# Kernel optimization log

Measured on AMD Instinct MI355X. Metric: run time of the kernel, lower is better.

The kernel has to match this reference:

```python
import jax, jax.numpy as jnp
import numpy as np

N = 10000          # nodes
E = 200000         # edges (avg degree 20)
LAT = 128          # latent dim
NEXP = 8           # experts
NTYPE = 95         # atom types (hard-coded 95x0e in module)
M0, M1, M2 = 128, 64, 32          # node/out irreps muls for l=0,1,2 (dim 480)
E0, E1, E2 = 64, 32, 16           # edge irreps muls (dim 240)
C0, C1, C2 = M0 + E0, M1 + E1, M2 + E2   # concat channels per l
T0 = M0 + M1 + M2                 # gate-input scalars: 128 scalars + 96 gates
AVG_NEIGH = 20.0


def setup_inputs() -> dict:
    key = jax.random.key(0)
    ks = jax.random.split(key, 32)
    r = lambda i, sh: jax.random.normal(ks[i], sh, dtype=jnp.float32)
    return {
        "latents": r(0, (E, LAT)),
        "node_features": r(1, (N, M0 + 3 * M1 + 5 * M2)),
        "edge_features": r(2, (E, E0 + 3 * E1 + 5 * E2)),
        "edge_vector": r(3, (E, 3)),
        "mole_globals": r(4, (LAT,)),
        "wigner_D1": r(5, (E, 3, 3)),
        "wigner_D2": r(6, (E, 5, 5)),
        "node_onehot": jax.nn.one_hot(jax.random.randint(ks[7], (N,), 0, NTYPE), NTYPE, dtype=jnp.float32),
        "Wg": r(8, (LAT, NEXP)),
        "Wm": r(9, (LAT, NEXP)),
        "W0_e": r(10, (NEXP, C0, T0)), "W0_s": r(11, (C0, T0)),
        "W1_e": r(12, (NEXP, C1, M1)), "W1_s": r(13, (C1, M1)),
        "W2_e": r(14, (NEXP, C2, M2)), "W2_s": r(15, (C2, M2)),
        "Wp0": r(16, (M0, M0)), "bp0": jnp.zeros((M0,), jnp.float32),
        "Wp1": r(17, (M1, M1)), "Wp2": r(18, (M2, M2)),
        "Wenv": r(19, (LAT, M0 + M1 + M2)),
        "Woh0": r(20, (M0, NTYPE)), "Woh1": r(21, (M1, NTYPE)), "Woh2": r(22, (M2, NTYPE)),
        "atom_type": jax.random.randint(ks[23], (N,), 0, NTYPE),
        "edge_index": jax.random.randint(ks[24], (2, E), 0, N),
        "active_edges": jnp.arange(E),
    }


def _mix(x, We, Ws, g):
    """Latent(expert)-conditioned per-l channel mixing: y = x @ (sum_e g_e W_e + W_shared).
    Loops over the small fixed expert count; never materializes per-edge weight matrices."""
    xm = x if x.ndim == 3 else x[:, :, None]           # [a, c, m]
    y = jnp.einsum('acm,co->aom', xm, Ws)
    for e in range(NEXP):
        y = y + g[:, e, None, None] * jnp.einsum('acm,co->aom', xm, We[e])
    y = y * float(1.0 / np.sqrt(xm.shape[1]))
    return y[:, :, 0] if x.ndim == 2 else y


def reference(latents, node_features, edge_features, edge_vector, mole_globals,
              wigner_D1, wigner_D2, node_onehot, Wg, Wm,
              W0_e, W0_s, W1_e, W1_s, W2_e, W2_s,
              Wp0, bp0, Wp1, Wp2, Wenv, Woh0, Woh1, Woh2,
              atom_type, edge_index, active_edges):
    edge_center = edge_index[0][active_edges]
    lat = latents[active_edges]
    # gather node features along edges, split irreps blocks
    xn = node_features[edge_center]                         # [Ea, 480]
    n0 = xn[:, :M0]
    n1 = xn[:, M0:M0 + 3 * M1].reshape(-1, M1, 3)
    n2 = xn[:, M0 + 3 * M1:].reshape(-1, M2, 5)
    e0 = edge_features[:, :E0]
    e1 = edge_features[:, E0:E0 + 3 * E1].reshape(-1, E1, 3)
    e2 = edge_features[:, E0 + 3 * E1:].reshape(-1, E2, 5)
    x0 = jnp.concatenate([n0, e0], axis=1)                  # [Ea, C0]
    x1 = jnp.concatenate([n1, e1], axis=1)                  # [Ea, C1, 3]
    x2 = jnp.concatenate([n2, e2], axis=1)                  # [Ea, C2, 5]
    # latent + molecular-global conditioned expert gates
    gates = jax.nn.softmax(lat @ Wg + mole_globals @ Wm, axis=-1)   # [Ea, NEXP]
    # SO(2)-style TP: rotate l>0 blocks into edge frame (Wigner-D), mix channels, rotate back
    x1r = jnp.einsum('amn,acn->acm', wigner_D1, x1)
    x2r = jnp.einsum('amn,acn->acm', wigner_D2, x2)
    t0 = _mix(x0, W0_e, W0_s, gates)                        # [Ea, T0]
    t1 = jnp.einsum('anm,aom->aon', wigner_D1, _mix(x1r, W1_e, W1_s, gates))
    t2 = jnp.einsum('anm,aom->aon', wigner_D2, _mix(x2r, W2_e, W2_s, gates))
    # Gate nonlinearity: silu scalars, sigmoid gates scale l>0 channels
    s = jax.nn.silu(t0[:, :M0])
    v1 = t1 * jax.nn.sigmoid(t0[:, M0:M0 + M1])[:, :, None]
    v2 = t2 * jax.nn.sigmoid(t0[:, M0 + M1:])[:, :, None]
    # lin_post: per-l equivariant linear (bias only on scalars), fan-in normalized
    s = s @ Wp0 * float(1.0 / np.sqrt(M0)) + bp0
    v1 = jnp.einsum('acm,co->aom', v1, Wp1) * float(1.0 / np.sqrt(M1))
    v2 = jnp.einsum('acm,co->aom', v2, Wp2) * float(1.0 / np.sqrt(M2))
    # E3ElementLinear: per-channel weights generated from latents
    w = lat @ Wenv * float(1.0 / np.sqrt(LAT))              # [Ea, M0+M1+M2]
    s = s * w[:, :M0]
    v1 = v1 * w[:, M0:M0 + M1, None]
    v2 = v2 * w[:, M0 + M1:, None]
    # scatter-reduce messages to nodes, normalize by rsqrt(avg_num_neighbors)
    norm = float(1.0 / np.sqrt(AVG_NEIGH))
    o0 = jax.ops.segment_sum(s, edge_center, num_segments=N) * norm
    o1 = jax.ops.segment_sum(v1, edge_center, num_segments=N) * norm
    o2 = jax.ops.segment_sum(v2, edge_center, num_segments=N) * norm
    # residual blend (res_update_params=0 -> u=sigmoid(0)=0.5), identity residual
    u = 0.5
    c_old = float(1.0 / np.sqrt(u * u + 1.0))
    c_new = u * c_old
    h0 = c_old * node_features[:, :M0] + c_new * o0
    h1 = c_old * node_features[:, M0:M0 + 3 * M1].reshape(N, M1, 3) + c_new * o1
    h2 = c_old * node_features[:, M0 + 3 * M1:].reshape(N, M2, 5) + c_new * o2
    # layer-onehot 'uvu' weighted TP with 95x0e, fan-in normalized, added residually
    invs = float(1.0 / np.sqrt(NTYPE))
    h0 = h0 + h0 * (node_onehot @ Woh0.T) * invs
    h1 = h1 + h1 * (node_onehot @ Woh1.T)[:, :, None] * invs
    h2 = h2 + h2 * (node_onehot @ Woh2.T)[:, :, None] * invs
    return jnp.concatenate([h0, h1.reshape(N, 3 * M1), h2.reshape(N, 5 * M2)], axis=1)
```

## Files before the change

kernel.cpp:

```cpp
#include <hip/hip_runtime.h>
#include <math.h>

namespace {

typedef __attribute__((ext_vector_type(8))) short short8;
typedef __attribute__((ext_vector_type(4))) float f32x4;

constexpr int kN   = 10000;
constexpr int kE   = 200000;
constexpr int kNT  = 95;
constexpr int kNFD = 480;

__device__ __forceinline__ ushort bf(float f) {
  union { float f; uint u; } c; c.f = f;
  uint r = c.u + 0x7FFF + ((c.u >> 16) & 1);
  return (ushort)(r >> 16);
}
__device__ __forceinline__ float fb(ushort u) {
  union { uint u; float f; } c; c.u = ((uint)u) << 16;
  return c.f;
}
__device__ __forceinline__ uint pk2(float a, float b) {
  return (uint)bf(a) | ((uint)bf(b) << 16);
}

__device__ __forceinline__ void fastbar() {
  asm volatile("s_waitcnt lgkmcnt(0)" ::: "memory");
  __builtin_amdgcn_s_barrier();
}

__device__ __forceinline__ void packone(int u, const float* We, const float* Ws,
                                        int expStride, int Kreal, int Nstride,
                                        int Nreal, int NT, int NKp, ushort* d) {
  int i = u & 7;
  int lane = (u >> 3) & 63;
  int rest = u >> 9;
  int kc = rest % NKp; rest /= NKp;
  int nt = rest % NT;
  int e  = rest / NT;
  int k = kc*32 + (lane >> 4)*8 + i;
  int n = nt*16 + (lane & 15);
  float v = 0.f;
  if (k < Kreal && n < Nreal) {
    const float* s = (Ws != nullptr && e == 8) ? Ws : (We + (size_t)e*expStride);
    v = s[(size_t)k*Nstride + n];
  }
  d[u] = bf(v);
}

constexpr int PK0   = 0;
constexpr int PK1   = 442368;
constexpr int PK2   = 497664;
constexpr int PKENV = 516096;
constexpr int PKP0  = 544768;
constexpr int PKP1  = 561152;
constexpr int PKP2  = 565248;
constexpr int PKTOT = 566272;

__global__ __launch_bounds__(256)
void pack_k(const float* __restrict__ W0e, const float* __restrict__ W0s,
            const float* __restrict__ W1e, const float* __restrict__ W1s,
            const float* __restrict__ W2e, const float* __restrict__ W2s,
            const float* __restrict__ Wenv, const float* __restrict__ Wp0,
            const float* __restrict__ Wp1, const float* __restrict__ Wp2,
            ushort* __restrict__ dst) {
  int gid = blockIdx.x*256 + threadIdx.x;
  if (gid >= PKTOT) return;
  if (gid < PK1)        packone(gid - PK0,   W0e, W0s, 192*224, 192, 224, 224, 16, 6, dst + PK0);
  else if (gid < PK2)   packone(gid - PK1,   W1e, W1s, 96*64,    96,  64,  64,  4, 3, dst + PK1);
  else if (gid < PKENV) packone(gid - PK2,   W2e, W2s, 48*32,    48,  32,  32,  2, 2, dst + PK2);
  else if (gid < PKP0)  packone(gid - PKENV, Wenv, nullptr, 0,  128, 224, 224, 14, 4, dst + PKENV);
  else if (gid < PKP1)  packone(gid - PKP0,  Wp0, nullptr, 0,   128, 128, 128,  8, 4, dst + PKP0);
  else if (gid < PKP2)  packone(gid - PKP1,  Wp1, nullptr, 0,    64,  64,  64,  4, 2, dst + PKP1);
  else                  packone(gid - PKP2,  Wp2, nullptr, 0,    32,  32,  32,  2, 1, dst + PKP2);
}

__global__ __launch_bounds__(64)
void mgl_k(const float* __restrict__ mgv, const float* __restrict__ Wm,
           float* __restrict__ mgl) {
  int x = threadIdx.x;
  if (x < 8) {
    float s = 0.f;
    for (int l = 0; l < 128; ++l) s += mgv[l]*Wm[l*8 + x];
    mgl[x] = s;
  }
}

__global__ __launch_bounds__(256)
void hist_k(const int* __restrict__ eidx, const int* __restrict__ act,
            int* __restrict__ counts) {
  int e = blockIdx.x*256 + threadIdx.x;
  if (e < kE) atomicAdd(&counts[eidx[act[e]]], 1);
}

__global__ __launch_bounds__(256)
void scan_k(const int* __restrict__ counts, int* __restrict__ rowptr,
            int* __restrict__ cursor) {
  __shared__ int part[256];
  const int t = threadIdx.x;
  const int start = t*40;
  int local = 0;
  for (int i = 0; i < 40; ++i) {
    int idx = start + i;
    if (idx < kN) local += counts[idx];
  }
  part[t] = local;
  __syncthreads();
  for (int ofs = 1; ofs < 256; ofs <<= 1) {
    int v = (t >= ofs) ? part[t - ofs] : 0;
    __syncthreads();
    part[t] += v;
    __syncthreads();
  }
  int run = part[t] - local;
  for (int i = 0; i < 40; ++i) {
    int idx = start + i;
    if (idx < kN) {
      rowptr[idx] = run;
      cursor[idx] = run;
      run += counts[idx];
    }
  }
  if (t == 255) rowptr[kN] = run;
}

__global__ __launch_bounds__(256)
void scatter_k(const int* __restrict__ eidx, const int* __restrict__ act,
               int* __restrict__ cursor, int* __restrict__ elist) {
  int e = blockIdx.x*256 + threadIdx.x;
  if (e < kE) {
    int n = eidx[act[e]];
    int pos = atomicAdd(&cursor[n], 1);
    elist[pos] = e;
  }
}

__global__ __launch_bounds__(256)
void prep_k(const float* __restrict__ latents, const float* __restrict__ nodef,
            const float* __restrict__ edgef, const float* __restrict__ mgl,
            const float* __restrict__ D1, const float* __restrict__ D2,
            const float* __restrict__ Wg,
            const int* __restrict__ eidx, const int* __restrict__ act,
            float* __restrict__ coefg,
            ushort* __restrict__ x0, ushort* __restrict__ x1r,
            ushort* __restrict__ x2r) {
  __shared__ int aidl[32], cenl[32];
  const int tid = threadIdx.x;
  const int base = blockIdx.x*32;

  if (tid < 32) {
    int a = act[base + tid];
    aidl[tid] = a;
    cenl[tid] = eidx[a];
  }
  __syncthreads();

  {
    int e = tid >> 3, x = tid & 7;
    const float* lat = latents + (size_t)aidl[e]*128;
    float s = mgl[x];
    for (int l = 0; l < 128; ++l) s += lat[l]*Wg[l*8 + x];
    float mx = s;
    mx = fmaxf(mx, __shfl_xor(mx, 1));
    mx = fmaxf(mx, __shfl_xor(mx, 2));
    mx = fmaxf(mx, __shfl_xor(mx, 4));
    float ex = __expf(s - mx);
    float sm = ex;
    sm += __shfl_xor(sm, 1);
    sm += __shfl_xor(sm, 2);
    sm += __shfl_xor(sm, 4);
    size_t a = base + e;
    coefg[a*9 + x] = ex/sm;
    if (x == 0) coefg[a*9 + 8] = 1.f;
  }

  for (int u = tid; u < 32*24; u += 256) {
    int e = u/24, g = u - e*24;
    int c0 = g*8;
    size_t a = base + e;
    const float* s = (g < 16) ? (nodef + (size_t)cenl[e]*kNFD + c0)
                              : (edgef + a*240 + (c0 - 128));
    float4 f0 = *(const float4*)s;
    float4 f1 = *(const float4*)(s + 4);
    uint4 o;
    o.x = pk2(f0.x, f0.y); o.y = pk2(f0.z, f0.w);
    o.z = pk2(f1.x, f1.y); o.w = pk2(f1.z, f1.w);
    *(uint4*)(x0 + a*192 + c0) = o;
  }

  for (int u = tid; u < 32*36; u += 256) {
    int e = u/36, r = u - e*36;
    int mm = r/12, g = r - mm*12;
    int c0 = g*8;
    size_t a = base + e;
    const float* dd = D1 + a*9 + mm*3;
    const float* s = (g < 8) ? (nodef + (size_t)cenl[e]*kNFD + 128 + c0*3)
                             : (edgef + a*240 + 64 + (c0 - 64)*3);
    float ld[24];
    #pragma unroll
    for (int q = 0; q < 6; ++q)
      *(float4*)(ld + q*4) = *(const float4*)(s + q*4);
    float d0 = dd[0], d1 = dd[1], d2 = dd[2];
    float ov[8];
    #pragma unroll
    for (int j = 0; j < 8; ++j)
      ov[j] = d0*ld[3*j] + d1*ld[3*j + 1] + d2*ld[3*j + 2];
    uint4 o;
    o.x = pk2(ov[0], ov[1]); o.y = pk2(ov[2], ov[3]);
    o.z = pk2(ov[4], ov[5]); o.w = pk2(ov[6], ov[7]);
    *(uint4*)(x1r + (a*3 + mm)*96 + c0) = o;
  }

  for (int u = tid; u < 32*40; u += 256) {
    int e = u/40, r = u - e*40;
    int mm = r >> 3, g = r & 7;
    int c0 = g*8;
    size_t a = base + e;
    uint4 o = {0u,0u,0u,0u};
    if (g < 6) {
      const float* dd = D2 + a*25 + mm*5;
      const float* s = (g < 4) ? (nodef + (size_t)cenl[e]*kNFD + 320 + c0*5)
                               : (edgef + a*240 + 160 + (c0 - 32)*5);
      float ld[40];
      #pragma unroll
      for (int q = 0; q < 10; ++q)
        *(float4*)(ld + q*4) = *(const float4*)(s + q*4);
      float d0 = dd[0], d1 = dd[1], d2 = dd[2], d3 = dd[3], d4 = dd[4];
      float ov[8];
      #pragma unroll
      for (int j = 0; j < 8; ++j)
        ov[j] = d0*ld[5*j] + d1*ld[5*j+1] + d2*ld[5*j+2] + d3*ld[5*j+3] + d4*ld[5*j+4];
      o.x = pk2(ov[0], ov[1]); o.y = pk2(ov[2], ov[3]);
      o.z = pk2(ov[4], ov[5]); o.w = pk2(ov[6], ov[7]);
    }
    *(uint4*)(x2r + (a*5 + mm)*64 + c0) = o;
  }
}

constexpr int gemm_smbytes(int K1, int NK, int N, int NEXP) {
  int LDA = K1 + 8;
  int NT = N/16;
  int a = 128*LDA*2;
  int b = NT*NK*1024;
  int u = a > b ? a : b;
  return u + (NEXP > 1 ? 128*NEXP*4 : 0);
}

template<int DIV, int K1, int NK, int N, int NEXP, int EPI, bool AF32>
__global__ __launch_bounds__(512)
void gemm_k(const ushort* __restrict__ A, const float* __restrict__ Af,
            const int* __restrict__ ridx, int strideA,
            const ushort* __restrict__ Bpk, const float* __restrict__ coefg,
            int rowsReal, float norm,
            ushort* __restrict__ outbf, const float* __restrict__ bias,
            const ushort* __restrict__ wenvbf, int WCOL) {
  constexpr int NT  = N/16;
  constexpr int CTW = NT/2;
  constexpr int LDA = K1 + 8;
  constexpr int ABYTES = 128*LDA*2;
  constexpr int BBYTES = NT*NK*1024;
  constexpr int UNI = (ABYTES > BBYTES) ? ABYTES : BBYTES;

  extern __shared__ char smraw[];
  ushort* Asm = (ushort*)smraw;
  float* coefsm = (float*)(smraw + UNI);

  const int tid = threadIdx.x;
  const int row0 = blockIdx.x*128;

  constexpr int C8 = K1/8;
  for (int u = tid; u < 128*C8; u += 512) {
    int r = u / C8, c8 = u - r*C8;
    int gr = row0 + r;
    uint4 v = {0u,0u,0u,0u};
    if (gr < rowsReal) {
      if constexpr (AF32) {
        const float* s = Af + (size_t)(ridx ? ridx[gr] : gr)*strideA + c8*8;
        float4 f0 = *(const float4*)s;
        float4 f1 = *(const float4*)(s + 4);
        v.x = pk2(f0.x, f0.y); v.y = pk2(f0.z, f0.w);
        v.z = pk2(f1.x, f1.y); v.w = pk2(f1.z, f1.w);
      } else {
        v = *(const uint4*)(A + (size_t)gr*strideA + c8*8);
      }
    }
    *(uint4*)(&Asm[r*LDA + c8*8]) = v;
  }
  if constexpr (NEXP > 1) {
    for (int u = tid; u < 128*NEXP; u += 512) {
      int r = u / NEXP, e = u - r*NEXP;
      int a = (row0 + r)/DIV;
      coefsm[r*NEXP + e] = coefg[(size_t)a*NEXP + e];
    }
  }
  __syncthreads();

  const int lane = tid & 63, wid = tid >> 6;
  const int cg = wid & 1, rg = wid >> 1;
  const int rbase = rg*32;
  const int lrow = lane & 15, lkb = lane >> 4;

  short8 af[2][NK];
  #pragma unroll
  for (int rt = 0; rt < 2; ++rt)
    #pragma unroll
    for (int kc = 0; kc < NK; ++kc)
      af[rt][kc] = *(const short8*)(&Asm[(rbase + rt*16 + lrow)*LDA + kc*32 + lkb*8]);

  f32x4 acc[2][CTW];
  #pragma unroll
  for (int rt = 0; rt < 2; ++rt)
    #pragma unroll
    for (int ct = 0; ct < CTW; ++ct)
      acc[rt][ct] = f32x4{0.f,0.f,0.f,0.f};

  __syncthreads();

  union BU { uint4 u; short8 s; };
  uint4* Bsm4 = (uint4*)smraw;
  const uint4* Bg4 = (const uint4*)Bpk;

  for (int e = 0; e < NEXP; ++e) {
    for (int u = tid; u < NT*NK*64; u += 512)
      Bsm4[u] = Bg4[(size_t)e*(NT*NK*64) + u];
    __syncthreads();

    if constexpr (NEXP > 1) {
      float cf[2][4];
      #pragma unroll
      for (int rt = 0; rt < 2; ++rt)
        #pragma unroll
        for (int q = 0; q < 4; ++q)
          cf[rt][q] = coefsm[(rbase + rt*16 + lkb*4 + q)*NEXP + e];
      #pragma unroll
      for (int ct = 0; ct < CTW; ++ct) {
        int nt = cg*CTW + ct;
        f32x4 z[2];
        z[0] = f32x4{0.f,0.f,0.f,0.f};
        z[1] = f32x4{0.f,0.f,0.f,0.f};
        #pragma unroll
        for (int kc = 0; kc < NK; ++kc) {
          BU b; b.u = Bsm4[(nt*NK + kc)*64 + lane];
          z[0] = __builtin_amdgcn_mfma_f32_16x16x32_bf16(af[0][kc], b.s, z[0], 0, 0, 0);
          z[1] = __builtin_amdgcn_mfma_f32_16x16x32_bf16(af[1][kc], b.s, z[1], 0, 0, 0);
        }
        #pragma unroll
        for (int q = 0; q < 4; ++q) {
          acc[0][ct][q] += cf[0][q]*z[0][q];
          acc[1][ct][q] += cf[1][q]*z[1][q];
        }
      }
    } else {
      #pragma unroll
      for (int ct = 0; ct < CTW; ++ct) {
        int nt = cg*CTW + ct;
        #pragma unroll
        for (int kc = 0; kc < NK; ++kc) {
          BU b; b.u = Bsm4[(nt*NK + kc)*64 + lane];
          acc[0][ct] = __builtin_amdgcn_mfma_f32_16x16x32_bf16(af[0][kc], b.s, acc[0][ct], 0, 0, 0);
          acc[1][ct] = __builtin_amdgcn_mfma_f32_16x16x32_bf16(af[1][kc], b.s, acc[1][ct], 0, 0, 0);
        }
      }
    }
    __syncthreads();
  }

  #pragma unroll
  for (int rt = 0; rt < 2; ++rt) {
    #pragma unroll
    for (int ct = 0; ct < CTW; ++ct) {
      #pragma unroll
      for (int q = 0; q < 4; ++q) {
        int gr = row0 + rbase + rt*16 + lkb*4 + q;
        if (gr >= rowsReal) continue;
        int o = (cg*CTW + ct)*16 + lrow;
        float val = acc[rt][ct][q]*norm;
        if constexpr (EPI == 0) {
          outbf[(size_t)gr*N + o] = bf(val);
        } else if constexpr (EPI == 1) {
          float av = (o < 128) ? (val/(1.f + __expf(-val)))
                               : (1.f/(1.f + __expf(-val)));
          outbf[(size_t)gr*N + o] = bf(av);
        } else {
          int a = gr/DIV;
          if (bias != nullptr) val += bias[o];
          float w = fb(wenvbf[(size_t)a*224 + WCOL + o]);
          val *= w*0.22360679774997896f;
          outbf[(size_t)gr*N + o] = bf(val);
        }
      }
    }
  }
}

constexpr int T0SMB = 55808;

template<int C>
__device__ __forceinline__ void t0_phase(int e, int tid, int lane, int cg,
                                         int rbase, int lkb,
                                         const short8 (&af)[2][6],
                                         f32x4 (&acc)[2][7],
                                         const float* coefsm,
                                         uint4* Bsm4, const uint4* Bg4,
                                         uint4& rg0, uint4& rg1, uint4& rg2) {
  fastbar();
  const bool hasNext = !(e == 8 && C == 3);
  if (hasNext) {
    int ne = e + (C == 3 ? 1 : 0);
    int nc = (C + 1) & 3;
    const uint4* s = Bg4 + (size_t)ne*6144 + (size_t)nc*1536;
    rg0 = s[tid]; rg1 = s[tid + 512]; rg2 = s[tid + 1024];
  }
  float cf[2][4];
  #pragma unroll
  for (int rt = 0; rt < 2; ++rt)
    #pragma unroll
    for (int q = 0; q < 4; ++q)
      cf[rt][q] = coefsm[(rbase + rt*16 + lkb*4 + q)*9 + e];
  union BU { uint4 u; short8 s; };
  const uint4* bb = Bsm4 + (C & 1)*1536;
  {
    f32x4 z0 = {0.f,0.f,0.f,0.f}, z1 = {0.f,0.f,0.f,0.f};
    #pragma unroll
    for (int kc = 0; kc < 6; ++kc) {
      BU b; b.u = bb[(cg*6 + kc)*64 + lane];
      z0 = __builtin_amdgcn_mfma_f32_16x16x32_bf16(af[0][kc], b.s, z0, 0, 0, 0);
      z1 = __builtin_amdgcn_mfma_f32_16x16x32_bf16(af[1][kc], b.s, z1, 0, 0, 0);
    }
    #pragma unroll
    for (int q = 0; q < 4; ++q) {
      acc[0][2*C][q] += cf[0][q]*z0[q];
      acc[1][2*C][q] += cf[1][q]*z1[q];
    }
  }
  if constexpr (2*C + 1 < 7) {
    f32x4 z0 = {0.f,0.f,0.f,0.f}, z1 = {0.f,0.f,0.f,0.f};
    #pragma unroll
    for (int kc = 0; kc < 6; ++kc) {
      BU b; b.u = bb[((2 + cg)*6 + kc)*64 + lane];
      z0 = __builtin_amdgcn_mfma_f32_16x16x32_bf16(af[0][kc], b.s, z0, 0, 0, 0);
      z1 = __builtin_amdgcn_mfma_f32_16x16x32_bf16(af[1][kc], b.s, z1, 0, 0, 0);
    }
    #pragma unroll
    for (int q = 0; q < 4; ++q) {
      acc[0][2*C + 1][q] += cf[0][q]*z0[q];
      acc[1][2*C + 1][q] += cf[1][q]*z1[q];
    }
  }
  fastbar();
  if (hasNext) {
    uint4* d = Bsm4 + ((C + 1) & 1)*1536;
    d[tid] = rg0; d[tid + 512] = rg1; d[tid + 1024] = rg2;
  }
}

__global__ __launch_bounds__(512, 2)
void t0c_k(const ushort* __restrict__ A, const ushort* __restrict__ Bpk,
           const float* __restrict__ coefg, ushort* __restrict__ outbf) {
  extern __shared__ char smraw[];
  ushort* Asm = (ushort*)smraw;
  float* coefsm = (float*)(smraw + 51200);
  uint4* Bsm4 = (uint4*)smraw;
  const uint4* Bg4 = (const uint4*)Bpk;

  const int tid = threadIdx.x;
  const int row0 = blockIdx.x*128;

  for (int u = tid; u < 128*24; u += 512) {
    int r = u/24, c8 = u - r*24;
    int gr = row0 + r;
    uint4 v = {0u,0u,0u,0u};
    if (gr < kE) v = *(const uint4*)(A + (size_t)gr*192 + c8*8);
    *(uint4*)(&Asm[r*200 + c8*8]) = v;
  }
  for (int u = tid; u < 128*9; u += 512) {
    int r = u/9, e = u - r*9;
    coefsm[r*9 + e] = coefg[(size_t)(row0 + r)*9 + e];
  }
  __syncthreads();

  const int lane = tid & 63, wid = tid >> 6;
  const int cg = wid & 1, rg = wid >> 1;
  const int rbase = rg*32;
  const int lrow = lane & 15, lkb = lane >> 4;

  short8 af[2][6];
  #pragma unroll
  for (int rt = 0; rt < 2; ++rt)
    #pragma unroll
    for (int kc = 0; kc < 6; ++kc)
      af[rt][kc] = *(const short8*)(&Asm[(rbase + rt*16 + lrow)*200 + kc*32 + lkb*8]);

  f32x4 acc[2][7];
  #pragma unroll
  for (int rt = 0; rt < 2; ++rt)
    #pragma unroll
    for (int ct = 0; ct < 7; ++ct)
      acc[rt][ct] = f32x4{0.f,0.f,0.f,0.f};

  __syncthreads();

  uint4 rg0, rg1, rg2;
  { const uint4* s = Bg4; rg0 = s[tid]; rg1 = s[tid + 512]; rg2 = s[tid + 1024]; }
  { uint4* d = Bsm4;      d[tid] = rg0; d[tid + 512] = rg1; d[tid + 1024] = rg2; }

  for (int e = 0; e < 9; ++e) {
    t0_phase<0>(e, tid, lane, cg, rbase, lkb, af, acc, coefsm, Bsm4, Bg4, rg0, rg1, rg2);
    t0_phase<1>(e, tid, lane, cg, rbase, lkb, af, acc, coefsm, Bsm4, Bg4, rg0, rg1, rg2);
    t0_phase<2>(e, tid, lane, cg, rbase, lkb, af, acc, coefsm, Bsm4, Bg4, rg0, rg1, rg2);
    t0_phase<3>(e, tid, lane, cg, rbase, lkb, af, acc, coefsm, Bsm4, Bg4, rg0, rg1, rg2);
  }

  #pragma unroll
  for (int rt = 0; rt < 2; ++rt) {
    #pragma unroll
    for (int ct = 0; ct < 7; ++ct) {
      #pragma unroll
      for (int q = 0; q < 4; ++q) {
        int gr = row0 + rbase + rt*16 + lkb*4 + q;
        if (gr >= kE) continue;
        int o = (2*ct + cg)*16 + lrow;
        float val = acc[rt][ct][q]*0.07216878364870323f;
        float av = (o < 128) ? (val/(1.f + __expf(-val)))
                             : (1.f/(1.f + __expf(-val)));
        outbf[(size_t)gr*224 + o] = bf(av);
      }
    }
  }
}

constexpr int ych_smbytes(int K1, int NK, int NT) {
  int a = 128*(K1 + 8)*2;
  int b = 2*NT*NK*1024;
  int u = a > b ? a : b;
  return u + 128*9*4;
}

template<int DIV, int K1, int NK, int NT>
__global__ __launch_bounds__(512, 2)
void ychunk_k(const ushort* __restrict__ A, const ushort* __restrict__ Bpk,
              const float* __restrict__ coefg, int rowsReal, float norm,
              ushort* __restrict__ outbf) {
  constexpr int CTW = NT/2;
  constexpr int N   = NT*16;
  constexpr int LDA = K1 + 8;
  constexpr int ABYTES = 128*LDA*2;
  constexpr int BBYTES = 2*NT*NK*1024;
  constexpr int UNI = (ABYTES > BBYTES) ? ABYTES : BBYTES;
  constexpr int NB4 = NT*NK*64;

  extern __shared__ char smraw[];
  ushort* Asm = (ushort*)smraw;
  float* coefsm = (float*)(smraw + UNI);
  uint4* Bsm4 = (uint4*)smraw;
  const uint4* Bg4 = (const uint4*)Bpk;

  const int tid = threadIdx.x;
  const int row0 = blockIdx.x*128;

  constexpr int C8 = K1/8;
  for (int u = tid; u < 128*C8; u += 512) {
    int r = u / C8, c8 = u - r*C8;
    int gr = row0 + r;
    uint4 v = {0u,0u,0u,0u};
    if (gr < rowsReal) v = *(const uint4*)(A + (size_t)gr*K1 + c8*8);
    *(uint4*)(&Asm[r*LDA + c8*8]) = v;
  }
  for (int u = tid; u < 128*9; u += 512) {
    int r = u/9, e = u - r*9;
    int a = (row0 + r)/DIV;
    coefsm[r*9 + e] = coefg[(size_t)a*9 + e];
  }
  __syncthreads();

  const int lane = tid & 63, wid = tid >> 6;
  const int cg = wid & 1, rg = wid >> 1;
  const int rbase = rg*32;
  const int lrow = lane & 15, lkb = lane >> 4;

  short8 af[2][NK];
  #pragma unroll
  for (int rt = 0; rt < 2; ++rt)
    #pragma unroll
    for (int kc = 0; kc < NK; ++kc)
      af[rt][kc] = *(const short8*)(&Asm[(rbase + rt*16 + lrow)*LDA + kc*32 + lkb*8]);

  f32x4 acc[2][CTW];
  #pragma unroll
  for (int rt = 0; rt < 2; ++rt)
    #pragma unroll
    for (int ct = 0; ct < CTW; ++ct)
      acc[rt][ct] = f32x4{0.f,0.f,0.f,0.f};

  __syncthreads();

  union BU { uint4 u; short8 s; };
  uint4 pf0, pf1;

  if (tid < NB4) pf0 = Bg4[tid];
  if constexpr (NB4 > 512) { if (tid + 512 < NB4) pf1 = Bg4[tid + 512]; }
  if (tid < NB4) Bsm4[tid] = pf0;
  if constexpr (NB4 > 512) { if (tid + 512 < NB4) Bsm4[tid + 512] = pf1; }

  for (int e = 0; e < 9; ++e) {
    fastbar();
    if (e + 1 < 9) {
      const uint4* s = Bg4 + (size_t)(e + 1)*NB4;
      if (tid < NB4) pf0 = s[tid];
      if constexpr (NB4 > 512) { if (tid + 512 < NB4) pf1 = s[tid + 512]; }
    }
    float cf[2][4];
    #pragma unroll
    for (int rt = 0; rt < 2; ++rt)
      #pragma unroll
      for (int q = 0; q < 4; ++q)
        cf[rt][q] = coefsm[(rbase + rt*16 + lkb*4 + q)*9 + e];
    const uint4* bb = Bsm4 + (e & 1)*NB4;
    #pragma unroll
    for (int ct = 0; ct < CTW; ++ct) {
      int nt = cg*CTW + ct;
      f32x4 z0 = {0.f,0.f,0.f,0.f}, z1 = {0.f,0.f,0.f,0.f};
      #pragma unroll
      for (int kc = 0; kc < NK; ++kc) {
        BU b; b.u = bb[(nt*NK + kc)*64 + lane];
        z0 = __builtin_amdgcn_mfma_f32_16x16x32_bf16(af[0][kc], b.s, z0, 0, 0, 0);
        z1 = __builtin_amdgcn_mfma_f32_16x16x32_bf16(af[1][kc], b.s, z1, 0, 0, 0);
      }
      #pragma unroll
      for (int q = 0; q < 4; ++q) {
        acc[0][ct][q] += cf[0][q]*z0[q];
        acc[1][ct][q] += cf[1][q]*z1[q];
      }
    }
    fastbar();
    if (e + 1 < 9) {
      uint4* d = Bsm4 + ((e + 1) & 1)*NB4;
      if (tid < NB4) d[tid] = pf0;
      if constexpr (NB4 > 512) { if (tid + 512 < NB4) d[tid + 512] = pf1; }
    }
  }

  #pragma unroll
  for (int rt = 0; rt < 2; ++rt) {
    #pragma unroll
    for (int ct = 0; ct < CTW; ++ct) {
      #pragma unroll
      for (int q = 0; q < 4; ++q) {
        int gr = row0 + rbase + rt*16 + lkb*4 + q;
        if (gr >= rowsReal) continue;
        int o = (cg*CTW + ct)*16 + lrow;
        outbf[(size_t)gr*N + o] = bf(acc[rt][ct][q]*norm);
      }
    }
  }
}

__global__ __launch_bounds__(256)
void mid_k(const ushort* __restrict__ y1, const ushort* __restrict__ y2,
           const ushort* __restrict__ t0act, const float* __restrict__ D1,
           const float* __restrict__ D2, ushort* __restrict__ v1,
           ushort* __restrict__ v2) {
  const int base = blockIdx.x*64;
  const int tid = threadIdx.x;

  for (int u = tid; u < 64*24; u += 256) {
    int e = u/24, r = u - e*24;
    int n = r >> 3, g = r & 7;
    int c0 = g*8;
    size_t a = base + e;
    const float* dd = D1 + a*9 + n*3;
    float d0 = dd[0], d1 = dd[1], d2 = dd[2];
    short8 m0 = *(const short8*)(y1 + ((size_t)a*3 + 0)*64 + c0);
    short8 m1 = *(const short8*)(y1 + ((size_t)a*3 + 1)*64 + c0);
    short8 m2 = *(const short8*)(y1 + ((size_t)a*3 + 2)*64 + c0);
    short8 gt = *(const short8*)(t0act + a*224 + 128 + c0);
    float ov[8];
    #pragma unroll
    for (int j = 0; j < 8; ++j) {
      float s = d0*fb((ushort)m0[j]) + d1*fb((ushort)m1[j]) + d2*fb((ushort)m2[j]);
      ov[j] = s*fb((ushort)gt[j]);
    }
    uint4 o;
    o.x = pk2(ov[0], ov[1]); o.y = pk2(ov[2], ov[3]);
    o.z = pk2(ov[4], ov[5]); o.w = pk2(ov[6], ov[7]);
    *(uint4*)(v1 + ((size_t)a*3 + n)*64 + c0) = o;
  }

  for (int u = tid; u < 64*20; u += 256) {
    int e = u/20, r = u - e*20;
    int n = r >> 2, g = r & 3;
    int c0 = g*8;
    size_t a = base + e;
    const float* dd = D2 + a*25 + n*5;
    short8 m0 = *(const short8*)(y2 + ((size_t)a*5 + 0)*32 + c0);
    short8 m1 = *(const short8*)(y2 + ((size_t)a*5 + 1)*32 + c0);
    short8 m2 = *(const short8*)(y2 + ((size_t)a*5 + 2)*32 + c0);
    short8 m3 = *(const short8*)(y2 + ((size_t)a*5 + 3)*32 + c0);
    short8 m4 = *(const short8*)(y2 + ((size_t)a*5 + 4)*32 + c0);
    short8 gt = *(const short8*)(t0act + a*224 + 192 + c0);
    float ov[8];
    #pragma unroll
    for (int j = 0; j < 8; ++j) {
      float s = dd[0]*fb((ushort)m0[j]) + dd[1]*fb((ushort)m1[j])
              + dd[2]*fb((ushort)m2[j]) + dd[3]*fb((ushort)m3[j])
              + dd[4]*fb((ushort)m4[j]);
      ov[j] = s*fb((ushort)gt[j]);
    }
    uint4 o;
    o.x = pk2(ov[0], ov[1]); o.y = pk2(ov[2], ov[3]);
    o.z = pk2(ov[4], ov[5]); o.w = pk2(ov[6], ov[7]);
    *(uint4*)(v2 + ((size_t)a*5 + n)*32 + c0) = o;
  }
}

__global__ __launch_bounds__(256)
void gather_k(const float* __restrict__ nodef, const float* __restrict__ onehot,
              const float* __restrict__ Woh0, const float* __restrict__ Woh1,
              const float* __restrict__ Woh2,
              const int* __restrict__ rowptr, const int* __restrict__ elist,
              const ushort* __restrict__ pe0, const ushort* __restrict__ pe1,
              const ushort* __restrict__ pe2, float* __restrict__ out) {
  __shared__ int tn;
  const int n = blockIdx.x;
  const int t = threadIdx.x;
  if (t < kNT && onehot[(size_t)n*kNT + t] > 0.5f) tn = t;
  __syncthreads();
  const int ty = tn;
  const int r0 = rowptr[n], r1 = rowptr[n + 1];
  const float c_old = 0.8944271909999159f;
  const float c_new = 0.4472135954999579f;
  const float invs  = 0.10259783520851541f;

  for (int j = t; j < kNFD; j += 256) {
    int kind, row_m, col;
    if (j < 128)       { kind = 0; row_m = 0; col = j; }
    else if (j < 320)  { int jj = j - 128; col = jj/3; row_m = jj - col*3; kind = 1; }
    else               { int jj = j - 320; col = jj/5; row_m = jj - col*5; kind = 2; }

    float s = 0.f;
    for (int d = r0; d < r1; ++d) {
      int e = elist[d];
      ushort v;
      if (kind == 0)      v = pe0[(size_t)e*128 + col];
      else if (kind == 1) v = pe1[((size_t)e*3 + row_m)*64 + col];
      else                v = pe2[((size_t)e*5 + row_m)*32 + col];
      s += fb(v);
    }

    size_t idx = (size_t)n*kNFD + j;
    float h = c_old*nodef[idx] + c_new*s;
    float f;
    if (j < 128)      f = Woh0[j*kNT + ty];
    else if (j < 320) f = Woh1[((j - 128)/3)*kNT + ty];
    else              f = Woh2[((j - 320)/5)*kNT + ty];
    out[idx] = h*(1.f + f*invs);
  }
}

constexpr size_t OFF_CNT  = 0;
constexpr size_t OFF_CUR  = 40000;
constexpr size_t OFF_RP   = 80000;
constexpr size_t OFF_EL   = 120064;
constexpr size_t OFF_PACK = 1000000;
constexpr size_t OFF_COEF = 19200000;
constexpr size_t OFF_MGL  = 26402304;
constexpr size_t OFF_X0   = 27202560;
constexpr size_t OFF_X1R  = 104027136;
constexpr size_t OFF_X2R  = 219264000;
constexpr size_t OFF_WENV = 347272192;
constexpr size_t OFF_T0A  = 436900864;
constexpr size_t OFF_Y1   = 526529536;
constexpr size_t OFF_Y2   = 603354112;

}

extern "C" void kernel_launch(void* const* d_in, const int* in_sizes, int n_in,
                              void* d_out, int out_size, void* d_ws, size_t ws_size,
                              hipStream_t stream) {
  (void)in_sizes; (void)n_in; (void)out_size; (void)ws_size;
  const float* latents = (const float*)d_in[0];
  const float* nodef   = (const float*)d_in[1];
  const float* edgef   = (const float*)d_in[2];
  const float* mg      = (const float*)d_in[4];
  const float* D1      = (const float*)d_in[5];
  const float* D2      = (const float*)d_in[6];
  const float* onehot  = (const float*)d_in[7];
  const float* Wg      = (const float*)d_in[8];
  const float* Wm      = (const float*)d_in[9];
  const float* W0e     = (const float*)d_in[10];
  const float* W0s     = (const float*)d_in[11];
  const float* W1e     = (const float*)d_in[12];
  const float* W1s     = (const float*)d_in[13];
  const float* W2e     = (const float*)d_in[14];
  const float* W2s     = (const float*)d_in[15];
  const float* Wp0     = (const float*)d_in[16];
  const float* bp0     = (const float*)d_in[17];
  const float* Wp1     = (const float*)d_in[18];
  const float* Wp2     = (const float*)d_in[19];
  const float* Wenv    = (const float*)d_in[20];
  const float* Woh0    = (const float*)d_in[21];
  const float* Woh1    = (const float*)d_in[22];
  const float* Woh2    = (const float*)d_in[23];
  const int* eidx      = (const int*)d_in[25];
  const int* act       = (const int*)d_in[26];

  char* ws = (char*)d_ws;
  int*    cnt   = (int*)(ws + OFF_CNT);
  int*    cur   = (int*)(ws + OFF_CUR);
  int*    rp    = (int*)(ws + OFF_RP);
  int*    el    = (int*)(ws + OFF_EL);
  ushort* pk    = (ushort*)(ws + OFF_PACK);
  float*  coef  = (float*)(ws + OFF_COEF);
  float*  mgl   = (float*)(ws + OFF_MGL);
  ushort* x0    = (ushort*)(ws + OFF_X0);
  ushort* x1r   = (ushort*)(ws + OFF_X1R);
  ushort* x2r   = (ushort*)(ws + OFF_X2R);
  ushort* wenv  = (ushort*)(ws + OFF_WENV);
  ushort* t0act = (ushort*)(ws + OFF_T0A);
  ushort* y1    = (ushort*)(ws + OFF_Y1);
  ushort* y2    = (ushort*)(ws + OFF_Y2);
  ushort* v1    = (ushort*)(ws + OFF_X0);
  ushort* v2    = (ushort*)(ws + OFF_X1R);
  ushort* pe1   = (ushort*)(ws + OFF_X2R);
  ushort* pe2   = (ushort*)(ws + OFF_Y1);
  ushort* pe0   = (ushort*)(ws + OFF_Y2);
  float*  out   = (float*)d_out;

  hipMemsetAsync(cnt, 0, kN*sizeof(int), stream);
  hist_k<<<(kE + 255)/256, 256, 0, stream>>>(eidx, act, cnt);
  scan_k<<<1, 256, 0, stream>>>(cnt, rp, cur);
  scatter_k<<<(kE + 255)/256, 256, 0, stream>>>(eidx, act, cur, el);

  pack_k<<<(PKTOT + 255)/256, 256, 0, stream>>>(W0e, W0s, W1e, W1s, W2e, W2s,
                                                Wenv, Wp0, Wp1, Wp2, pk);
  mgl_k<<<1, 64, 0, stream>>>(mg, Wm, mgl);

  prep_k<<<kE/32, 256, 0, stream>>>(latents, nodef, edgef, mgl, D1, D2, Wg,
                                    eidx, act, coef, x0, x1r, x2r);

  {
    hipFuncSetAttribute((const void*)t0c_k,
                        hipFuncAttributeMaxDynamicSharedMemorySize, T0SMB);
    t0c_k<<<1563, 512, T0SMB, stream>>>(x0, pk + PK0, coef, t0act);
  }
  {
    auto kp = gemm_k<1,128,4,224,1,0,true>;
    int smb = gemm_smbytes(128,4,224,1);
    hipFuncSetAttribute((const void*)kp, hipFuncAttributeMaxDynamicSharedMemorySize, smb);
    kp<<<1563, 512, smb, stream>>>(
        nullptr, latents, act, 128, pk + PKENV, nullptr, kE, 0.08838834764831845f,
        wenv, nullptr, nullptr, 0);
  }
  {
    auto kp = ychunk_k<3,96,3,4>;
    int smb = ych_smbytes(96,3,4);
    hipFuncSetAttribute((const void*)kp, hipFuncAttributeMaxDynamicSharedMemorySize, smb);
    kp<<<4688, 512, smb, stream>>>(
        x1r, pk + PK1, coef, 3*kE, 0.10206207261596577f, y1);
  }
  {
    auto kp = ychunk_k<5,64,2,2>;
    int smb = ych_smbytes(64,2,2);
    hipFuncSetAttribute((const void*)kp, hipFuncAttributeMaxDynamicSharedMemorySize, smb);
    kp<<<7813, 512, smb, stream>>>(
        x2r, pk + PK2, coef, 5*kE, 0.14433756729740643f, y2);
  }

  mid_k<<<kE/64, 256, 0, stream>>>(y1, y2, t0act, D1, D2, v1, v2);

  {
    auto kp = gemm_k<1,128,4,128,1,2,false>;
    int smb = gemm_smbytes(128,4,128,1);
    hipFuncSetAttribute((const void*)kp, hipFuncAttributeMaxDynamicSharedMemorySize, smb);
    kp<<<1563, 512, smb, stream>>>(
        t0act, nullptr, nullptr, 224, pk + PKP0, nullptr, kE, 0.08838834764831845f,
        pe0, bp0, wenv, 0);
  }
  {
    auto kp = gemm_k<3,64,2,64,1,2,false>;
    int smb = gemm_smbytes(64,2,64,1);
    hipFuncSetAttribute((const void*)kp, hipFuncAttributeMaxDynamicSharedMemorySize, smb);
    kp<<<4688, 512, smb, stream>>>(
        v1, nullptr, nullptr, 64, pk + PKP1, nullptr, 3*kE, 0.125f,
        pe1, nullptr, wenv, 128);
  }
  {
    auto kp = gemm_k<5,32,1,32,1,2,false>;
    int smb = gemm_smbytes(32,1,32,1);
    hipFuncSetAttribute((const void*)kp, hipFuncAttributeMaxDynamicSharedMemorySize, smb);
    kp<<<7813, 512, smb, stream>>>(
        v2, nullptr, nullptr, 32, pk + PKP2, nullptr, 5*kE, 0.17677669529663687f,
        pe2, nullptr, wenv, 192);
  }

  gather_k<<<kN, 256, 0, stream>>>(nodef, onehot, Woh0, Woh1, Woh2,
                                   rp, el, pe0, pe1, pe2, out);
}
```

Before: 1.381 ms.

## Remap warps so each B fragment feeds four row tiles in t0 and y-chunk GEMMs

```diff
diff --git a/kernel.cpp b/kernel.cpp
--- a/kernel.cpp
+++ b/kernel.cpp
@@ -398,8 +398,8 @@
 template<int C>
 __device__ __forceinline__ void t0_phase(int e, int tid, int lane, int cg,
                                          int rbase, int lkb,
-                                         const short8 (&af)[2][6],
-                                         f32x4 (&acc)[2][7],
+                                         const short8 (&af)[4][6],
+                                         f32x4 (&acc)[4][4],
                                          const float* coefsm,
                                          uint4* Bsm4, const uint4* Bg4,
                                          uint4& rg0, uint4& rg1, uint4& rg2) {
@@ -411,42 +411,29 @@
     const uint4* s = Bg4 + (size_t)ne*6144 + (size_t)nc*1536;
     rg0 = s[tid]; rg1 = s[tid + 512]; rg2 = s[tid + 1024];
   }
-  float cf[2][4];
-  #pragma unroll
-  for (int rt = 0; rt < 2; ++rt)
+  float cf[4][4];
+  #pragma unroll
+  for (int rt = 0; rt < 4; ++rt)
     #pragma unroll
     for (int q = 0; q < 4; ++q)
       cf[rt][q] = coefsm[(rbase + rt*16 + lkb*4 + q)*9 + e];
   union BU { uint4 u; short8 s; };
   const uint4* bb = Bsm4 + (C & 1)*1536;
-  {
-    f32x4 z0 = {0.f,0.f,0.f,0.f}, z1 = {0.f,0.f,0.f,0.f};
-    #pragma unroll
-    for (int kc = 0; kc < 6; ++kc) {
-      BU b; b.u = bb[(cg*6 + kc)*64 + lane];
-      z0 = __builtin_amdgcn_mfma_f32_16x16x32_bf16(af[0][kc], b.s, z0, 0, 0, 0);
-      z1 = __builtin_amdgcn_mfma_f32_16x16x32_bf16(af[1][kc], b.s, z1, 0, 0, 0);
-    }
-    #pragma unroll
-    for (int q = 0; q < 4; ++q) {
-      acc[0][2*C][q] += cf[0][q]*z0[q];
-      acc[1][2*C][q] += cf[1][q]*z1[q];
-    }
-  }
-  if constexpr (2*C + 1 < 7) {
-    f32x4 z0 = {0.f,0.f,0.f,0.f}, z1 = {0.f,0.f,0.f,0.f};
-    #pragma unroll
-    for (int kc = 0; kc < 6; ++kc) {
-      BU b; b.u = bb[((2 + cg)*6 + kc)*64 + lane];
-      z0 = __builtin_amdgcn_mfma_f32_16x16x32_bf16(af[0][kc], b.s, z0, 0, 0, 0);
-      z1 = __builtin_amdgcn_mfma_f32_16x16x32_bf16(af[1][kc], b.s, z1, 0, 0, 0);
-    }
-    #pragma unroll
-    for (int q = 0; q < 4; ++q) {
-      acc[0][2*C + 1][q] += cf[0][q]*z0[q];
-      acc[1][2*C + 1][q] += cf[1][q]*z1[q];
-    }
-  }
+  f32x4 z[4];
+  #pragma unroll
+  for (int rt = 0; rt < 4; ++rt) z[rt] = f32x4{0.f,0.f,0.f,0.f};
+  #pragma unroll
+  for (int kc = 0; kc < 6; ++kc) {
+    BU b; b.u = bb[(cg*6 + kc)*64 + lane];
+    #pragma unroll
+    for (int rt = 0; rt < 4; ++rt)
+      z[rt] = __builtin_amdgcn_mfma_f32_16x16x32_bf16(af[rt][kc], b.s, z[rt], 0, 0, 0);
+  }
+  #pragma unroll
+  for (int rt = 0; rt < 4; ++rt)
+    #pragma unroll
+    for (int q = 0; q < 4; ++q)
+      acc[rt][C][q] += cf[rt][q]*z[rt][q];
   fastbar();
   if (hasNext) {
     uint4* d = Bsm4 + ((C + 1) & 1)*1536;
@@ -454,7 +441,7 @@
   }
 }
 
-__global__ __launch_bounds__(512, 2)
+__global__ __launch_bounds__(512, 1)
 void t0c_k(const ushort* __restrict__ A, const ushort* __restrict__ Bpk,
            const float* __restrict__ coefg, ushort* __restrict__ outbf) {
   extern __shared__ char smraw[];
@@ -480,23 +467,23 @@
   __syncthreads();
 
   const int lane = tid & 63, wid = tid >> 6;
-  const int cg = wid & 1, rg = wid >> 1;
-  const int rbase = rg*32;
+  const int cg = wid & 3, rg = wid >> 2;
+  const int rbase = rg*64;
   const int lrow = lane & 15, lkb = lane >> 4;
 
-  short8 af[2][6];
-  #pragma unroll
-  for (int rt = 0; rt < 2; ++rt)
+  short8 af[4][6];
+  #pragma unroll
+  for (int rt = 0; rt < 4; ++rt)
     #pragma unroll
     for (int kc = 0; kc < 6; ++kc)
       af[rt][kc] = *(const short8*)(&Asm[(rbase + rt*16 + lrow)*200 + kc*32 + lkb*8]);
 
-  f32x4 acc[2][7];
-  #pragma unroll
-  for (int rt = 0; rt < 2; ++rt)
-    #pragma unroll
-    for (int ct = 0; ct < 7; ++ct)
-      acc[rt][ct] = f32x4{0.f,0.f,0.f,0.f};
+  f32x4 acc[4][4];
+  #pragma unroll
+  for (int rt = 0; rt < 4; ++rt)
+    #pragma unroll
+    for (int C = 0; C < 4; ++C)
+      acc[rt][C] = f32x4{0.f,0.f,0.f,0.f};
 
   __syncthreads();
 
@@ -512,15 +499,17 @@
   }
 
   #pragma unroll
-  for (int rt = 0; rt < 2; ++rt) {
-    #pragma unroll
-    for (int ct = 0; ct < 7; ++ct) {
+  for (int rt = 0; rt < 4; ++rt) {
+    #pragma unroll
+    for (int C = 0; C < 4; ++C) {
+      int nt = 4*C + cg;
+      if (nt >= 14) continue;
+      int o = nt*16 + lrow;
       #pragma unroll
       for (int q = 0; q < 4; ++q) {
         int gr = row0 + rbase + rt*16 + lkb*4 + q;
         if (gr >= kE) continue;
-        int o = (2*ct + cg)*16 + lrow;
-        float val = acc[rt][ct][q]*0.07216878364870323f;
+        float val = acc[rt][C][q]*0.07216878364870323f;
         float av = (o < 128) ? (val/(1.f + __expf(-val)))
                              : (1.f/(1.f + __expf(-val)));
         outbf[(size_t)gr*224 + o] = bf(av);
@@ -536,12 +525,13 @@
   return u + 128*9*4;
 }
 
-template<int DIV, int K1, int NK, int NT>
+template<int DIV, int K1, int NK, int NT, int CGN>
 __global__ __launch_bounds__(512, 2)
 void ychunk_k(const ushort* __restrict__ A, const ushort* __restrict__ Bpk,
               const float* __restrict__ coefg, int rowsReal, float norm,
               ushort* __restrict__ outbf) {
-  constexpr int CTW = NT/2;
+  constexpr int RT  = CGN;
+  constexpr int CTW = NT/CGN;
   constexpr int N   = NT*16;
   constexpr int LDA = K1 + 8;
   constexpr int ABYTES = 128*LDA*2;
@@ -574,20 +564,20 @@
   __syncthreads();
 
   const int lane = tid & 63, wid = tid >> 6;
-  const int cg = wid & 1, rg = wid >> 1;
-  const int rbase = rg*32;
+  const int cg = wid & (CGN - 1), rg = wid/CGN;
+  const int rbase = rg*(16*RT);
   const int lrow = lane & 15, lkb = lane >> 4;
 
-  short8 af[2][NK];
-  #pragma unroll
-  for (int rt = 0; rt < 2; ++rt)
+  short8 af[RT][NK];
+  #pragma unroll
+  for (int rt = 0; rt < RT; ++rt)
     #pragma unroll
     for (int kc = 0; kc < NK; ++kc)
       af[rt][kc] = *(const short8*)(&Asm[(rbase + rt*16 + lrow)*LDA + kc*32 + lkb*8]);
 
-  f32x4 acc[2][CTW];
-  #pragma unroll
-  for (int rt = 0; rt < 2; ++rt)
+  f32x4 acc[RT][CTW];
+  #pragma unroll
+  for (int rt = 0; rt < RT; ++rt)
     #pragma unroll
     for (int ct = 0; ct < CTW; ++ct)
       acc[rt][ct] = f32x4{0.f,0.f,0.f,0.f};
@@ -609,9 +599,9 @@
       if (tid < NB4) pf0 = s[tid];
       if constexpr (NB4 > 512) { if (tid + 512 < NB4) pf1 = s[tid + 512]; }
     }
-    float cf[2][4];
-    #pragma unroll
-    for (int rt = 0; rt < 2; ++rt)
+    float cf[RT][4];
+    #pragma unroll
+    for (int rt = 0; rt < RT; ++rt)
       #pragma unroll
       for (int q = 0; q < 4; ++q)
         cf[rt][q] = coefsm[(rbase + rt*16 + lkb*4 + q)*9 + e];
@@ -619,18 +609,21 @@
     #pragma unroll
     for (int ct = 0; ct < CTW; ++ct) {
       int nt = cg*CTW + ct;
-      f32x4 z0 = {0.f,0.f,0.f,0.f}, z1 = {0.f,0.f,0.f,0.f};
+      f32x4 z[RT];
+      #pragma unroll
+      for (int rt = 0; rt < RT; ++rt) z[rt] = f32x4{0.f,0.f,0.f,0.f};
       #pragma unroll
       for (int kc = 0; kc < NK; ++kc) {
         BU b; b.u = bb[(nt*NK + kc)*64 + lane];
-        z0 = __builtin_amdgcn_mfma_f32_16x16x32_bf16(af[0][kc], b.s, z0, 0, 0, 0);
-        z1 = __builtin_amdgcn_mfma_f32_16x16x32_bf16(af[1][kc], b.s, z1, 0, 0, 0);
+        #pragma unroll
+        for (int rt = 0; rt < RT; ++rt)
+          z[rt] = __builtin_amdgcn_mfma_f32_16x16x32_bf16(af[rt][kc], b.s, z[rt], 0, 0, 0);
       }
       #pragma unroll
-      for (int q = 0; q < 4; ++q) {
-        acc[0][ct][q] += cf[0][q]*z0[q];
-        acc[1][ct][q] += cf[1][q]*z1[q];
-      }
+      for (int rt = 0; rt < RT; ++rt)
+        #pragma unroll
+        for (int q = 0; q < 4; ++q)
+          acc[rt][ct][q] += cf[rt][q]*z[rt][q];
     }
     fastbar();
     if (e + 1 < 9) {
@@ -641,7 +634,7 @@
   }
 
   #pragma unroll
-  for (int rt = 0; rt < 2; ++rt) {
+  for (int rt = 0; rt < RT; ++rt) {
     #pragma unroll
     for (int ct = 0; ct < CTW; ++ct) {
       #pragma unroll
@@ -852,14 +845,14 @@
         wenv, nullptr, nullptr, 0);
   }
   {
-    auto kp = ychunk_k<3,96,3,4>;
+    auto kp = ychunk_k<3,96,3,4,4>;
     int smb = ych_smbytes(96,3,4);
     hipFuncSetAttribute((const void*)kp, hipFuncAttributeMaxDynamicSharedMemorySize, smb);
     kp<<<4688, 512, smb, stream>>>(
         x1r, pk + PK1, coef, 3*kE, 0.10206207261596577f, y1);
   }
   {
-    auto kp = ychunk_k<5,64,2,2>;
+    auto kp = ychunk_k<5,64,2,2,2>;
     int smb = ych_smbytes(64,2,2);
     hipFuncSetAttribute((const void*)kp, hipFuncAttributeMaxDynamicSharedMemorySize, smb);
     kp<<<7813, 512, smb, stream>>>(
```

After: 1.798 ms. +30.2%, slower.

## Fuse scalar post-projection GEMM into t0c kernel epilogue

Applied to the files above, without the earlier changes.

```diff
diff --git a/kernel.cpp b/kernel.cpp
--- a/kernel.cpp
+++ b/kernel.cpp
@@ -456,7 +456,9 @@
 
 __global__ __launch_bounds__(512, 2)
 void t0c_k(const ushort* __restrict__ A, const ushort* __restrict__ Bpk,
-           const float* __restrict__ coefg, ushort* __restrict__ outbf) {
+           const ushort* __restrict__ Bp0, const float* __restrict__ coefg,
+           const float* __restrict__ bp0f, const ushort* __restrict__ wenvbf,
+           ushort* __restrict__ t0act, ushort* __restrict__ pe0) {
   extern __shared__ char smraw[];
   ushort* Asm = (ushort*)smraw;
   float* coefsm = (float*)(smraw + 51200);
@@ -511,19 +513,67 @@
     t0_phase<3>(e, tid, lane, cg, rbase, lkb, af, acc, coefsm, Bsm4, Bg4, rg0, rg1, rg2);
   }
 
+  ushort* A2 = (ushort*)smraw;
   #pragma unroll
   for (int rt = 0; rt < 2; ++rt) {
     #pragma unroll
     for (int ct = 0; ct < 7; ++ct) {
+      int o = (2*ct + cg)*16 + lrow;
+      #pragma unroll
+      for (int q = 0; q < 4; ++q) {
+        int rloc = rbase + rt*16 + lkb*4 + q;
+        int gr = row0 + rloc;
+        float val = acc[rt][ct][q]*0.07216878364870323f;
+        if (o < 128) {
+          A2[rloc*136 + o] = bf(val/(1.f + __expf(-val)));
+        } else if (gr < kE) {
+          t0act[(size_t)gr*224 + o] = bf(1.f/(1.f + __expf(-val)));
+        }
+      }
+    }
+  }
+  fastbar();
+
+  short8 af2[2][4];
+  #pragma unroll
+  for (int rt = 0; rt < 2; ++rt)
+    #pragma unroll
+    for (int kc = 0; kc < 4; ++kc)
+      af2[rt][kc] = *(const short8*)(&A2[(rbase + rt*16 + lrow)*136 + kc*32 + lkb*8]);
+
+  union BU { uint4 u; short8 s; };
+  const uint4* Bg0 = (const uint4*)Bp0;
+  f32x4 acc2[2][4];
+  #pragma unroll
+  for (int rt = 0; rt < 2; ++rt)
+    #pragma unroll
+    for (int ct = 0; ct < 4; ++ct)
+      acc2[rt][ct] = f32x4{0.f,0.f,0.f,0.f};
+
+  #pragma unroll
+  for (int ct = 0; ct < 4; ++ct) {
+    int nt = cg*4 + ct;
+    #pragma unroll
+    for (int kc = 0; kc < 4; ++kc) {
+      BU b; b.u = Bg0[(nt*4 + kc)*64 + lane];
+      acc2[0][ct] = __builtin_amdgcn_mfma_f32_16x16x32_bf16(af2[0][kc], b.s, acc2[0][ct], 0, 0, 0);
+      acc2[1][ct] = __builtin_amdgcn_mfma_f32_16x16x32_bf16(af2[1][kc], b.s, acc2[1][ct], 0, 0, 0);
+    }
+  }
+
+  #pragma unroll
+  for (int rt = 0; rt < 2; ++rt) {
+    #pragma unroll
+    for (int ct = 0; ct < 4; ++ct) {
+      int o = (cg*4 + ct)*16 + lrow;
+      float bia = bp0f[o];
       #pragma unroll
       for (int q = 0; q < 4; ++q) {
         int gr = row0 + rbase + rt*16 + lkb*4 + q;
         if (gr >= kE) continue;
-        int o = (2*ct + cg)*16 + lrow;
-        float val = acc[rt][ct][q]*0.07216878364870323f;
-        float av = (o < 128) ? (val/(1.f + __expf(-val)))
-                             : (1.f/(1.f + __expf(-val)));
-        outbf[(size_t)gr*224 + o] = bf(av);
+        float v = acc2[rt][ct][q]*0.08838834764831845f + bia;
+        v *= fb(wenvbf[(size_t)gr*224 + o])*0.22360679774997896f;
+        pe0[(size_t)gr*128 + o] = bf(v);
       }
     }
   }
@@ -766,6 +816,7 @@
 constexpr size_t OFF_MGL  = 26402304;
 constexpr size_t OFF_X0   = 27202560;
 constexpr size_t OFF_X1R  = 104027136;
+constexpr size_t OFF_PE0  = 168031232;
 constexpr size_t OFF_X2R  = 219264000;
 constexpr size_t OFF_WENV = 347272192;
 constexpr size_t OFF_T0A  = 436900864;
@@ -821,9 +872,9 @@
   ushort* y2    = (ushort*)(ws + OFF_Y2);
   ushort* v1    = (ushort*)(ws + OFF_X0);
   ushort* v2    = (ushort*)(ws + OFF_X1R);
+  ushort* pe0   = (ushort*)(ws + OFF_PE0);
   ushort* pe1   = (ushort*)(ws + OFF_X2R);
   ushort* pe2   = (ushort*)(ws + OFF_Y1);
-  ushort* pe0   = (ushort*)(ws + OFF_Y2);
   float*  out   = (float*)d_out;
 
   hipMemsetAsync(cnt, 0, kN*sizeof(int), stream);
@@ -838,11 +889,6 @@
   prep_k<<<kE/32, 256, 0, stream>>>(latents, nodef, edgef, mgl, D1, D2, Wg,
                                     eidx, act, coef, x0, x1r, x2r);
 
-  {
-    hipFuncSetAttribute((const void*)t0c_k,
-                        hipFuncAttributeMaxDynamicSharedMemorySize, T0SMB);
-    t0c_k<<<1563, 512, T0SMB, stream>>>(x0, pk + PK0, coef, t0act);
-  }
   {
     auto kp = gemm_k<1,128,4,224,1,0,true>;
     int smb = gemm_smbytes(128,4,224,1);
@@ -866,16 +912,15 @@
         x2r, pk + PK2, coef, 5*kE, 0.14433756729740643f, y2);
   }
 
+  {
+    hipFuncSetAttribute((const void*)t0c_k,
+                        hipFuncAttributeMaxDynamicSharedMemorySize, T0SMB);
+    t0c_k<<<1563, 512, T0SMB, stream>>>(x0, pk + PK0, pk + PKP0, coef,
+                                        bp0, wenv, t0act, pe0);
+  }
+
   mid_k<<<kE/64, 256, 0, stream>>>(y1, y2, t0act, D1, D2, v1, v2);
 
-  {
-    auto kp = gemm_k<1,128,4,128,1,2,false>;
-    int smb = gemm_smbytes(128,4,128,1);
-    hipFuncSetAttribute((const void*)kp, hipFuncAttributeMaxDynamicSharedMemorySize, smb);
-    kp<<<1563, 512, smb, stream>>>(
-        t0act, nullptr, nullptr, 224, pk + PKP0, nullptr, kE, 0.08838834764831845f,
-        pe0, bp0, wenv, 0);
-  }
   {
     auto kp = gemm_k<3,64,2,64,1,2,false>;
     int smb = gemm_smbytes(64,2,64,1);
```

After: 1.371 ms. No clear change (-0.7%).
